# Optimization experiments

Measured on AMD Instinct MI355X. Metric: run time of the kernel, lower is better.

## Reference

```python
import jax, jax.numpy as jnp
import numpy as np

N_NODES = 8192
IN_DIM = 128
HIDDEN = 128
N_EDGES = 262144


def gcn_layer(x, W, b, src, dst, n):
    # GCNConv: h = D^{-1/2}(A+I)D^{-1/2} (x @ W) + b, with added self-loops
    h = x @ W  # [n, out]
    loop = jnp.arange(n, dtype=src.dtype)
    s = jnp.concatenate([src, loop])
    d = jnp.concatenate([dst, loop])
    deg = jax.ops.segment_sum(jnp.ones_like(s, dtype=h.dtype), d, num_segments=n)
    dinv = jax.lax.rsqrt(deg)  # deg >= 1 due to self-loops
    norm = dinv[s] * dinv[d]  # [E+n]
    msg = h[s] * norm[:, None]
    out = jax.ops.segment_sum(msg, d, num_segments=n)
    return out + b


def setup_inputs() -> dict:
    key = jax.random.key(0)
    ks = jax.random.split(key, 10)
    g = 1.0 / np.sqrt(HIDDEN)
    inp = {
        "x": jax.random.normal(ks[0], (N_NODES, IN_DIM), dtype=jnp.float32),
        "edge_index": jax.random.randint(ks[1], (2, N_EDGES), 0, N_NODES, dtype=jnp.int32),
        "W1": jax.random.normal(ks[2], (IN_DIM, HIDDEN), dtype=jnp.float32) * (1.0 / np.sqrt(IN_DIM)),
        "b1": jnp.zeros((HIDDEN,), dtype=jnp.float32),
        "W2": jax.random.normal(ks[3], (HIDDEN, HIDDEN), dtype=jnp.float32) * g,
        "b2": jnp.zeros((HIDDEN,), dtype=jnp.float32),
        "W_out": jax.random.normal(ks[4], (HIDDEN, HIDDEN), dtype=jnp.float32) * g,
        "b_out": jnp.zeros((HIDDEN,), dtype=jnp.float32),
        "W_edge": jax.random.normal(ks[5], (2 * HIDDEN,), dtype=jnp.float32) * (1.0 / np.sqrt(2 * HIDDEN)),
        "b_edge": jnp.zeros((), dtype=jnp.float32),
    }
    return inp


def reference(x, edge_index, W1, b1, W2, b2, W_out, b_out, W_edge, b_edge):
    src, dst = edge_index[0], edge_index[1]
    n = x.shape[0]
    h = jax.nn.relu(gcn_layer(x, W1, b1, src, dst, n))
    h = jax.nn.relu(gcn_layer(h, W2, b2, src, dst, n))
    h = h @ W_out + b_out  # [n, hidden]
    # edge_proj(cat(x_i, x_j)) decomposes: logits[i,j] = h_i.w_i + h_j.w_j + b
    w_i, w_j = W_edge[:HIDDEN], W_edge[HIDDEN:]
    a = h @ w_i  # [n]
    c = h @ w_j  # [n]
    edge_logits = a[:, None] + c[None, :] + b_edge  # [n, n]
    return edge_logits
```

## Files before the change

kernel.cpp:

```cpp
#include <hip/hip_runtime.h>

#define NN 8192
#define NE 262144
#define DIM 128
#define BCAP 128

typedef float f32x4 __attribute__((ext_vector_type(4)));

__device__ __forceinline__ float4 f4fma(float s, float4 w, float4 acc) {
    acc.x = fmaf(s, w.x, acc.x);
    acc.y = fmaf(s, w.y, acc.y);
    acc.z = fmaf(s, w.z, acc.z);
    acc.w = fmaf(s, w.w, acc.w);
    return acc;
}
__device__ __forceinline__ float f4dot(float4 a, float4 b) {
    return fmaf(a.x, b.x, fmaf(a.y, b.y, fmaf(a.z, b.z, a.w * b.w)));
}

__global__ __launch_bounds__(256) void init_kernel(const float* __restrict__ Wout,
                                                   const float* __restrict__ bout,
                                                   const float* __restrict__ we,
                                                   const float* __restrict__ bedge,
                                                   int* __restrict__ cnt,
                                                   float* __restrict__ u,
                                                   float* __restrict__ v,
                                                   float* __restrict__ beta) {
    int k = threadIdx.x;
    if (blockIdx.x < 32) {
        cnt[blockIdx.x * 256 + k] = 0;
        return;
    }
    if (k < DIM) {
        const float4* W4 = (const float4*)(Wout + (k << 7));
        const float4* we4 = (const float4*)we;
        float su = 0.f, sv = 0.f;
#pragma unroll
        for (int j = 0; j < 32; ++j) {
            float4 w = W4[j];
            su += f4dot(w, we4[j]);
            sv += f4dot(w, we4[32 + j]);
        }
        u[k] = su;
        v[k] = sv;
    }
    __shared__ float red[256];
    red[k] = (k < DIM) ? bout[k] * we[k] : 0.f;
    __syncthreads();
    for (int off = 128; off >= 1; off >>= 1) {
        if (k < off) red[k] += red[k + off];
        __syncthreads();
    }
    float b0 = red[0];
    __syncthreads();
    red[k] = (k < DIM) ? bout[k] * we[DIM + k] : 0.f;
    __syncthreads();
    for (int off = 128; off >= 1; off >>= 1) {
        if (k < off) red[k] += red[k + off];
        __syncthreads();
    }
    if (k == 0) {
        beta[0] = b0 + bedge[0];
        beta[1] = red[0];
    }
}

__global__ __launch_bounds__(256) void scatter_kernel(const int* __restrict__ src,
                                                      const int* __restrict__ dst,
                                                      int* __restrict__ cnt,
                                                      int* __restrict__ bucket) {
    int e = blockIdx.x * 256 + threadIdx.x;
    int d = dst[e];
    int p = atomicAdd(&cnt[d], 1);
    if (p < BCAP) bucket[(d << 7) + p] = src[e];
}

__global__ __launch_bounds__(256) void gemm_pre(const float* __restrict__ X,
                                                const float* __restrict__ W,
                                                const int* __restrict__ cnt,
                                                float* __restrict__ G) {
    __shared__ float4 Wl[128 * 32];
    __shared__ float4 Xl[32 * 32];
    int tid = threadIdx.x;
    int rbase = blockIdx.x * 32;

    const float4* W4 = (const float4*)W;
#pragma unroll
    for (int i = 0; i < 16; ++i) Wl[i * 256 + tid] = W4[i * 256 + tid];
    const float4* X4 = (const float4*)(X + rbase * DIM);
#pragma unroll
    for (int i = 0; i < 4; ++i) Xl[i * 256 + tid] = X4[i * 256 + tid];
    __syncthreads();

    int tx = tid & 31;
    int ty = tid >> 5;
    float4 acc[4];
#pragma unroll
    for (int i = 0; i < 4; ++i) acc[i] = make_float4(0.f, 0.f, 0.f, 0.f);

    for (int k4 = 0; k4 < 32; ++k4) {
        float4 w0 = Wl[(k4 * 4 + 0) * 32 + tx];
        float4 w1 = Wl[(k4 * 4 + 1) * 32 + tx];
        float4 w2 = Wl[(k4 * 4 + 2) * 32 + tx];
        float4 w3 = Wl[(k4 * 4 + 3) * 32 + tx];
#pragma unroll
        for (int i = 0; i < 4; ++i) {
            float4 xv = Xl[(ty * 4 + i) * 32 + k4];
            acc[i] = f4fma(xv.x, w0, acc[i]);
            acc[i] = f4fma(xv.y, w1, acc[i]);
            acc[i] = f4fma(xv.z, w2, acc[i]);
            acc[i] = f4fma(xv.w, w3, acc[i]);
        }
    }

    float4* G4 = (float4*)G;
#pragma unroll
    for (int i = 0; i < 4; ++i) {
        int r = rbase + ty * 4 + i;
        float dv = rsqrtf((float)(cnt[r] + 1));
        float4 o = acc[i];
        o.x *= dv; o.y *= dv; o.z *= dv; o.w *= dv;
        G4[r * 32 + tx] = o;
    }
}

__global__ __launch_bounds__(256) void agg_gemm(const float* __restrict__ G1,
                                                const int* __restrict__ cnt,
                                                const int* __restrict__ bucket,
                                                const float* __restrict__ b1,
                                                const float* __restrict__ W2,
                                                float* __restrict__ G2) {
    __shared__ float4 Wl[128 * 32];
    __shared__ float4 Xl[32 * 32];
    int tid = threadIdx.x;
    int rbase = blockIdx.x * 32;
    int w = tid >> 6;
    int lane = tid & 63;

    const float2* G12 = (const float2*)G1;
    int deg[8], i0[8], i1[8];
    float dv[8];
    float2 acc[8];
    int nb = rbase + w * 8;
#pragma unroll
    for (int j = 0; j < 8; ++j) {
        int n = nb + j;
        deg[j] = cnt[n];
        dv[j] = rsqrtf((float)(deg[j] + 1));
        i0[j] = bucket[(n << 7) + lane];
        i1[j] = bucket[(n << 7) + 64 + lane];
        acc[j] = G12[n * 64 + lane];
    }

    const float4* W4 = (const float4*)W2;
#pragma unroll
    for (int i = 0; i < 16; ++i) Wl[i * 256 + tid] = W4[i * 256 + tid];

    int m = max(max(max(deg[0], deg[1]), max(deg[2], deg[3])),
                max(max(deg[4], deg[5]), max(deg[6], deg[7])));
    for (int e = 0; e < m; ++e) {
        int lo = e & 63;
        bool hi = e >= 64;
#pragma unroll
        for (int j = 0; j < 8; ++j) {
            int s = __shfl(hi ? i1[j] : i0[j], lo);
            bool val = e < deg[j];
            s = val ? s : 0;
            float wt = val ? 1.f : 0.f;
            float2 t = G12[s * 64 + lane];
            acc[j].x = fmaf(t.x, wt, acc[j].x);
            acc[j].y = fmaf(t.y, wt, acc[j].y);
        }
    }

    const float2* B2 = (const float2*)b1;
    float2 bb = B2[lane];
    float2* Xl2 = (float2*)Xl;
#pragma unroll
    for (int j = 0; j < 8; ++j) {
        float2 o;
        o.x = fmaxf(fmaf(acc[j].x, dv[j], bb.x), 0.f) * dv[j];
        o.y = fmaxf(fmaf(acc[j].y, dv[j], bb.y), 0.f) * dv[j];
        Xl2[(w * 8 + j) * 64 + lane] = o;
    }
    __syncthreads();

    int tx = tid & 31;
    int ty = tid >> 5;
    float4 accg[4];
#pragma unroll
    for (int i = 0; i < 4; ++i) accg[i] = make_float4(0.f, 0.f, 0.f, 0.f);

    for (int k4 = 0; k4 < 32; ++k4) {
        float4 w0 = Wl[(k4 * 4 + 0) * 32 + tx];
        float4 w1 = Wl[(k4 * 4 + 1) * 32 + tx];
        float4 w2 = Wl[(k4 * 4 + 2) * 32 + tx];
        float4 w3 = Wl[(k4 * 4 + 3) * 32 + tx];
#pragma unroll
        for (int i = 0; i < 4; ++i) {
            float4 xv = Xl[(ty * 4 + i) * 32 + k4];
            accg[i] = f4fma(xv.x, w0, accg[i]);
            accg[i] = f4fma(xv.y, w1, accg[i]);
            accg[i] = f4fma(xv.z, w2, accg[i]);
            accg[i] = f4fma(xv.w, w3, accg[i]);
        }
    }

    float4* G4 = (float4*)G2;
#pragma unroll
    for (int i = 0; i < 4; ++i) {
        int r = rbase + ty * 4 + i;
        G4[r * 32 + tx] = accg[i];
    }
}

__global__ __launch_bounds__(256) void agg_head(const float* __restrict__ G2,
                                                const int* __restrict__ cnt,
                                                const int* __restrict__ bucket,
                                                const float* __restrict__ b2,
                                                const float* __restrict__ u,
                                                const float* __restrict__ v,
                                                const float* __restrict__ beta,
                                                float* __restrict__ a,
                                                float* __restrict__ c) {
    int node = blockIdx.x * 4 + (threadIdx.x >> 6);
    int lane = threadIdx.x & 63;
    const float2* G22 = (const float2*)G2;

    int deg = cnt[node];
    float dv = rsqrtf((float)(deg + 1));
    int i0 = bucket[(node << 7) + lane];
    int i1 = bucket[(node << 7) + 64 + lane];

    float2 p0 = G22[node * 64 + lane];
    float2 p1 = {0.f, 0.f}, p2 = {0.f, 0.f}, p3 = {0.f, 0.f};

    int d4 = deg & ~3;
    for (int e = 0; e < d4; e += 4) {
        int s0 = __shfl((e + 0) >= 64 ? i1 : i0, (e + 0) & 63);
        int s1 = __shfl((e + 1) >= 64 ? i1 : i0, (e + 1) & 63);
        int s2 = __shfl((e + 2) >= 64 ? i1 : i0, (e + 2) & 63);
        int s3 = __shfl((e + 3) >= 64 ? i1 : i0, (e + 3) & 63);
        float2 t0 = G22[s0 * 64 + lane];
        float2 t1 = G22[s1 * 64 + lane];
        float2 t2 = G22[s2 * 64 + lane];
        float2 t3 = G22[s3 * 64 + lane];
        p0.x += t0.x; p0.y += t0.y;
        p1.x += t1.x; p1.y += t1.y;
        p2.x += t2.x; p2.y += t2.y;
        p3.x += t3.x; p3.y += t3.y;
    }
    for (int e = d4; e < deg; ++e) {
        int s = __shfl(e >= 64 ? i1 : i0, e & 63);
        float2 t = G22[s * 64 + lane];
        p0.x += t.x; p0.y += t.y;
    }
    float yx = (p0.x + p1.x) + (p2.x + p3.x);
    float yy = (p0.y + p1.y) + (p2.y + p3.y);

    const float2* B2 = (const float2*)b2;
    float2 bb = B2[lane];
    float h0 = fmaxf(fmaf(yx, dv, bb.x), 0.f);
    float h1 = fmaxf(fmaf(yy, dv, bb.y), 0.f);

    float2 uu = ((const float2*)u)[lane];
    float2 vv = ((const float2*)v)[lane];
    float pa = h0 * uu.x + h1 * uu.y;
    float pc = h0 * vv.x + h1 * vv.y;
#pragma unroll
    for (int off = 32; off >= 1; off >>= 1) {
        pa += __shfl_xor(pa, off);
        pc += __shfl_xor(pc, off);
    }
    if (lane == 0) {
        a[node] = pa + beta[0];
        c[node] = pc + beta[1];
    }
}

__global__ __launch_bounds__(256) void out_kernel(const float* __restrict__ a,
                                                  const float* __restrict__ c,
                                                  f32x4* __restrict__ out) {
    const f32x4* c4 = (const f32x4*)c;
    size_t base = (size_t)blockIdx.x * 1024 + threadIdx.x;
#pragma unroll
    for (int q = 0; q < 4; ++q) {
        size_t idx = base + q * 256;
        int i = (int)(idx >> 11);
        int j4 = (int)(idx & 2047);
        f32x4 r = c4[j4] + a[i];
        __builtin_nontemporal_store(r, out + idx);
    }
}

extern "C" void kernel_launch(void* const* d_in, const int* in_sizes, int n_in,
                              void* d_out, int out_size, void* d_ws, size_t ws_size,
                              hipStream_t stream) {
    const float* x    = (const float*)d_in[0];
    const int*   ei   = (const int*)d_in[1];
    const float* W1   = (const float*)d_in[2];
    const float* b1   = (const float*)d_in[3];
    const float* W2   = (const float*)d_in[4];
    const float* b2   = (const float*)d_in[5];
    const float* Wout = (const float*)d_in[6];
    const float* bout = (const float*)d_in[7];
    const float* We   = (const float*)d_in[8];
    const float* bedge= (const float*)d_in[9];
    const int* src = ei;
    const int* dst = ei + NE;

    int* cnt     = (int*)d_ws;
    int* bucket  = cnt + NN;
    float* u     = (float*)(bucket + NN * BCAP);
    float* v     = u + DIM;
    float* beta  = v + DIM;
    float* g1    = beta + 16;
    float* g2    = g1 + NN * DIM;
    float* av    = g2 + NN * DIM;
    float* cv    = av + NN;

    float* out = (float*)d_out;

    init_kernel<<<33, 256, 0, stream>>>(Wout, bout, We, bedge, cnt, u, v, beta);
    scatter_kernel<<<NE / 256, 256, 0, stream>>>(src, dst, cnt, bucket);
    gemm_pre<<<NN / 32, 256, 0, stream>>>(x, W1, cnt, g1);
    agg_gemm<<<NN / 32, 256, 0, stream>>>(g1, cnt, bucket, b1, W2, g2);
    agg_head<<<NN / 4, 256, 0, stream>>>(g2, cnt, bucket, b2, u, v, beta, av, cv);
    out_kernel<<<(NN * NN / 4) / 1024, 256, 0, stream>>>(av, cv, (f32x4*)out);
}
```

Before: 121.1 us.

## Split fused aggregate+GEMM into per-node gather kernel and separate GEMM

The fused agg_gemm kernel handled 8 nodes per wave in lockstep up to the maximum degree. It is replaced by a gather_scale kernel with one wave per node and 4-way unrolled independent loads, followed by a plain gemm_mid kernel that reads an intermediate buffer s2. The init work is also restructured: zeroing gets its own small kernel and the u/v/beta computation is folded into the scatter kernel as an extra block. Nontemporal loads and stores are added for bucket and the G buffers. This removes divergence and padding waste in the gather, at the cost of an extra launch and an extra 4 MB round trip through memory.

```diff
diff --git a/kernel.cpp b/kernel.cpp
--- a/kernel.cpp
+++ b/kernel.cpp
@@ -6,6 +6,7 @@
 #define BCAP 128
 
 typedef float f32x4 __attribute__((ext_vector_type(4)));
+typedef float f32x2 __attribute__((ext_vector_type(2)));
 
 __device__ __forceinline__ float4 f4fma(float s, float4 w, float4 acc) {
     acc.x = fmaf(s, w.x, acc.x);
@@ -18,17 +19,27 @@
     return fmaf(a.x, b.x, fmaf(a.y, b.y, fmaf(a.z, b.z, a.w * b.w)));
 }
 
-__global__ __launch_bounds__(256) void init_kernel(const float* __restrict__ Wout,
-                                                   const float* __restrict__ bout,
-                                                   const float* __restrict__ we,
-                                                   const float* __restrict__ bedge,
-                                                   int* __restrict__ cnt,
-                                                   float* __restrict__ u,
-                                                   float* __restrict__ v,
-                                                   float* __restrict__ beta) {
+__global__ __launch_bounds__(256) void zero_kernel(int* __restrict__ cnt) {
+    cnt[blockIdx.x * 256 + threadIdx.x] = 0;
+}
+
+__global__ __launch_bounds__(256) void scatter_uv(const int* __restrict__ src,
+                                                  const int* __restrict__ dst,
+                                                  int* __restrict__ cnt,
+                                                  int* __restrict__ bucket,
+                                                  const float* __restrict__ Wout,
+                                                  const float* __restrict__ bout,
+                                                  const float* __restrict__ we,
+                                                  const float* __restrict__ bedge,
+                                                  float* __restrict__ u,
+                                                  float* __restrict__ v,
+                                                  float* __restrict__ beta) {
     int k = threadIdx.x;
-    if (blockIdx.x < 32) {
-        cnt[blockIdx.x * 256 + k] = 0;
+    if (blockIdx.x < 1024) {
+        int e = blockIdx.x * 256 + k;
+        int d = dst[e];
+        int p = atomicAdd(&cnt[d], 1);
+        if (p < BCAP) bucket[(d << 7) + p] = src[e];
         return;
     }
     if (k < DIM) {
@@ -65,20 +76,10 @@
     }
 }
 
-__global__ __launch_bounds__(256) void scatter_kernel(const int* __restrict__ src,
-                                                      const int* __restrict__ dst,
-                                                      int* __restrict__ cnt,
-                                                      int* __restrict__ bucket) {
-    int e = blockIdx.x * 256 + threadIdx.x;
-    int d = dst[e];
-    int p = atomicAdd(&cnt[d], 1);
-    if (p < BCAP) bucket[(d << 7) + p] = src[e];
-}
-
 __global__ __launch_bounds__(256) void gemm_pre(const float* __restrict__ X,
                                                 const float* __restrict__ W,
                                                 const int* __restrict__ cnt,
-                                                float* __restrict__ G) {
+                                                f32x4* __restrict__ G) {
     __shared__ float4 Wl[128 * 32];
     __shared__ float4 Xl[32 * 32];
     int tid = threadIdx.x;
@@ -113,83 +114,84 @@
         }
     }
 
-    float4* G4 = (float4*)G;
 #pragma unroll
     for (int i = 0; i < 4; ++i) {
         int r = rbase + ty * 4 + i;
         float dv = rsqrtf((float)(cnt[r] + 1));
-        float4 o = acc[i];
-        o.x *= dv; o.y *= dv; o.z *= dv; o.w *= dv;
-        G4[r * 32 + tx] = o;
-    }
-}
-
-__global__ __launch_bounds__(256) void agg_gemm(const float* __restrict__ G1,
-                                                const int* __restrict__ cnt,
-                                                const int* __restrict__ bucket,
-                                                const float* __restrict__ b1,
-                                                const float* __restrict__ W2,
-                                                float* __restrict__ G2) {
+        f32x4 o = {acc[i].x * dv, acc[i].y * dv, acc[i].z * dv, acc[i].w * dv};
+        __builtin_nontemporal_store(o, G + r * 32 + tx);
+    }
+}
+
+__global__ __launch_bounds__(256) void gather_scale(const float* __restrict__ G1,
+                                                    const int* __restrict__ cnt,
+                                                    const int* __restrict__ bucket,
+                                                    const float* __restrict__ b1,
+                                                    f32x2* __restrict__ S2) {
+    int node = blockIdx.x * 4 + (threadIdx.x >> 6);
+    int lane = threadIdx.x & 63;
+    const float2* G12 = (const float2*)G1;
+
+    int deg = cnt[node];
+    float dv = rsqrtf((float)(deg + 1));
+    int i0 = __builtin_nontemporal_load(bucket + (node << 7) + lane);
+    int i1 = __builtin_nontemporal_load(bucket + (node << 7) + 64 + lane);
+
+    float2 p0 = G12[node * 64 + lane];
+    float2 p1 = {0.f, 0.f}, p2 = {0.f, 0.f}, p3 = {0.f, 0.f};
+
+    int d4 = deg & ~3;
+    for (int e = 0; e < d4; e += 4) {
+        int s0 = __shfl((e + 0) >= 64 ? i1 : i0, (e + 0) & 63);
+        int s1 = __shfl((e + 1) >= 64 ? i1 : i0, (e + 1) & 63);
+        int s2 = __shfl((e + 2) >= 64 ? i1 : i0, (e + 2) & 63);
+        int s3 = __shfl((e + 3) >= 64 ? i1 : i0, (e + 3) & 63);
+        float2 t0 = G12[s0 * 64 + lane];
+        float2 t1 = G12[s1 * 64 + lane];
+        float2 t2 = G12[s2 * 64 + lane];
+        float2 t3 = G12[s3 * 64 + lane];
+        p0.x += t0.x; p0.y += t0.y;
+        p1.x += t1.x; p1.y += t1.y;
+        p2.x += t2.x; p2.y += t2.y;
+        p3.x += t3.x; p3.y += t3.y;
+    }
+    for (int e = d4; e < deg; ++e) {
+        int s = __shfl(e >= 64 ? i1 : i0, e & 63);
+        float2 t = G12[s * 64 + lane];
+        p0.x += t.x; p0.y += t.y;
+    }
+    float yx = (p0.x + p1.x) + (p2.x + p3.x);
+    float yy = (p0.y + p1.y) + (p2.y + p3.y);
+
+    const float2* B2 = (const float2*)b1;
+    float2 bb = B2[lane];
+    f32x2 o;
+    o.x = fmaxf(fmaf(yx, dv, bb.x), 0.f) * dv;
+    o.y = fmaxf(fmaf(yy, dv, bb.y), 0.f) * dv;
+    __builtin_nontemporal_store(o, S2 + node * 64 + lane);
+}
+
+__global__ __launch_bounds__(256) void gemm_mid(const float* __restrict__ X,
+                                                const float* __restrict__ W,
+                                                f32x4* __restrict__ G) {
     __shared__ float4 Wl[128 * 32];
     __shared__ float4 Xl[32 * 32];
     int tid = threadIdx.x;
     int rbase = blockIdx.x * 32;
-    int w = tid >> 6;
-    int lane = tid & 63;
-
-    const float2* G12 = (const float2*)G1;
-    int deg[8], i0[8], i1[8];
-    float dv[8];
-    float2 acc[8];
-    int nb = rbase + w * 8;
-#pragma unroll
-    for (int j = 0; j < 8; ++j) {
-        int n = nb + j;
-        deg[j] = cnt[n];
-        dv[j] = rsqrtf((float)(deg[j] + 1));
-        i0[j] = bucket[(n << 7) + lane];
-        i1[j] = bucket[(n << 7) + 64 + lane];
-        acc[j] = G12[n * 64 + lane];
-    }
-
-    const float4* W4 = (const float4*)W2;
+
+    const float4* W4 = (const float4*)W;
 #pragma unroll
     for (int i = 0; i < 16; ++i) Wl[i * 256 + tid] = W4[i * 256 + tid];
-
-    int m = max(max(max(deg[0], deg[1]), max(deg[2], deg[3])),
-                max(max(deg[4], deg[5]), max(deg[6], deg[7])));
-    for (int e = 0; e < m; ++e) {
-        int lo = e & 63;
-        bool hi = e >= 64;
-#pragma unroll
-        for (int j = 0; j < 8; ++j) {
-            int s = __shfl(hi ? i1[j] : i0[j], lo);
-            bool val = e < deg[j];
-            s = val ? s : 0;
-            float wt = val ? 1.f : 0.f;
-            float2 t = G12[s * 64 + lane];
-            acc[j].x = fmaf(t.x, wt, acc[j].x);
-            acc[j].y = fmaf(t.y, wt, acc[j].y);
-        }
-    }
-
-    const float2* B2 = (const float2*)b1;
-    float2 bb = B2[lane];
-    float2* Xl2 = (float2*)Xl;
-#pragma unroll
-    for (int j = 0; j < 8; ++j) {
-        float2 o;
-        o.x = fmaxf(fmaf(acc[j].x, dv[j], bb.x), 0.f) * dv[j];
-        o.y = fmaxf(fmaf(acc[j].y, dv[j], bb.y), 0.f) * dv[j];
-        Xl2[(w * 8 + j) * 64 + lane] = o;
-    }
+    const float4* X4 = (const float4*)(X + rbase * DIM);
+#pragma unroll
+    for (int i = 0; i < 4; ++i) Xl[i * 256 + tid] = X4[i * 256 + tid];
     __syncthreads();
 
     int tx = tid & 31;
     int ty = tid >> 5;
-    float4 accg[4];
-#pragma unroll
-    for (int i = 0; i < 4; ++i) accg[i] = make_float4(0.f, 0.f, 0.f, 0.f);
+    float4 acc[4];
+#pragma unroll
+    for (int i = 0; i < 4; ++i) acc[i] = make_float4(0.f, 0.f, 0.f, 0.f);
 
     for (int k4 = 0; k4 < 32; ++k4) {
         float4 w0 = Wl[(k4 * 4 + 0) * 32 + tx];
@@ -199,18 +201,18 @@
 #pragma unroll
         for (int i = 0; i < 4; ++i) {
             float4 xv = Xl[(ty * 4 + i) * 32 + k4];
-            accg[i] = f4fma(xv.x, w0, accg[i]);
-            accg[i] = f4fma(xv.y, w1, accg[i]);
-            accg[i] = f4fma(xv.z, w2, accg[i]);
-            accg[i] = f4fma(xv.w, w3, accg[i]);
+            acc[i] = f4fma(xv.x, w0, acc[i]);
+            acc[i] = f4fma(xv.y, w1, acc[i]);
+            acc[i] = f4fma(xv.z, w2, acc[i]);
+            acc[i] = f4fma(xv.w, w3, acc[i]);
         }
     }
 
-    float4* G4 = (float4*)G2;
 #pragma unroll
     for (int i = 0; i < 4; ++i) {
         int r = rbase + ty * 4 + i;
-        G4[r * 32 + tx] = accg[i];
+        f32x4 o = {acc[i].x, acc[i].y, acc[i].z, acc[i].w};
+        __builtin_nontemporal_store(o, G + r * 32 + tx);
     }
 }
 
@@ -229,8 +231,8 @@
 
     int deg = cnt[node];
     float dv = rsqrtf((float)(deg + 1));
-    int i0 = bucket[(node << 7) + lane];
-    int i1 = bucket[(node << 7) + 64 + lane];
+    int i0 = __builtin_nontemporal_load(bucket + (node << 7) + lane);
+    int i1 = __builtin_nontemporal_load(bucket + (node << 7) + 64 + lane);
 
     float2 p0 = G22[node * 64 + lane];
     float2 p1 = {0.f, 0.f}, p2 = {0.f, 0.f}, p3 = {0.f, 0.f};
@@ -315,16 +317,19 @@
     float* v     = u + DIM;
     float* beta  = v + DIM;
     float* g1    = beta + 16;
-    float* g2    = g1 + NN * DIM;
+    float* s2    = g1 + NN * DIM;
+    float* g2    = s2 + NN * DIM;
     float* av    = g2 + NN * DIM;
     float* cv    = av + NN;
 
     float* out = (float*)d_out;
 
-    init_kernel<<<33, 256, 0, stream>>>(Wout, bout, We, bedge, cnt, u, v, beta);
-    scatter_kernel<<<NE / 256, 256, 0, stream>>>(src, dst, cnt, bucket);
-    gemm_pre<<<NN / 32, 256, 0, stream>>>(x, W1, cnt, g1);
-    agg_gemm<<<NN / 32, 256, 0, stream>>>(g1, cnt, bucket, b1, W2, g2);
+    zero_kernel<<<32, 256, 0, stream>>>(cnt);
+    scatter_uv<<<1025, 256, 0, stream>>>(src, dst, cnt, bucket,
+                                         Wout, bout, We, bedge, u, v, beta);
+    gemm_pre<<<NN / 32, 256, 0, stream>>>(x, W1, cnt, (f32x4*)g1);
+    gather_scale<<<NN / 4, 256, 0, stream>>>(g1, cnt, bucket, b1, (f32x2*)s2);
+    gemm_mid<<<NN / 32, 256, 0, stream>>>(s2, W2, (f32x4*)g2);
     agg_head<<<NN / 4, 256, 0, stream>>>(g2, cnt, bucket, b2, u, v, beta, av, cv);
     out_kernel<<<(NN * NN / 4) / 1024, 256, 0, stream>>>(av, cv, (f32x4*)out);
 }
```

Result: faster. 112.8 us (-6.9%).
